# Kernel optimization log

Hardware: AMD Instinct MI355X
Metric: run time of the kernel (lower is better)

The kernel has to match this reference:

```python
import jax, jax.numpy as jnp
import numpy as np

B, S, H, F, G = 8, 2048, 1024, 4096, 128
EPS = 1e-5


def setup_inputs() -> dict:
    key = jax.random.key(0)
    ks = jax.random.split(key, 8)
    x = jax.random.normal(ks[0], (B, S, H), dtype=jnp.float32)
    ln_gamma = jnp.ones((H,), jnp.float32)
    ln_beta = jnp.zeros((H,), jnp.float32)
    # int8-style quantized weights stored as int32 in [0, 256) with zero-point 128
    fc1_q = jax.random.randint(ks[1], (H, F), 0, 256, dtype=jnp.int32)
    fc2_q = jax.random.randint(ks[2], (F, H), 0, 256, dtype=jnp.int32)
    # per-group scales (one scale per 128 rows of K, per output column)
    fc1_scales = jax.random.uniform(ks[3], (H // G, F), jnp.float32) * 0.02 + 0.001
    fc2_scales = jax.random.uniform(ks[4], (F // G, H), jnp.float32) * 0.02 + 0.001
    fc1_bias = jax.random.normal(ks[5], (F,), jnp.float32) * 0.02
    fc2_bias = jax.random.normal(ks[6], (H,), jnp.float32) * 0.02
    return {"x": x, "ln_gamma": ln_gamma, "ln_beta": ln_beta,
            "fc1_q": fc1_q, "fc1_scales": fc1_scales, "fc1_bias": fc1_bias,
            "fc2_q": fc2_q, "fc2_scales": fc2_scales, "fc2_bias": fc2_bias}


def _dequant(q, scales, g):
    # q: [K, N] int, scales: [K//g, N]; zero-point 128 symmetric int8 scheme
    K, N = q.shape
    w = (q.astype(jnp.float32) - 128.0).reshape(K // g, g, N) * scales[:, None, :]
    return w.reshape(K, N)


def reference(x, ln_gamma, ln_beta, fc1_q, fc1_scales, fc1_bias, fc2_q, fc2_scales, fc2_bias):
    residual = x
    # LayerNorm over last dim
    mu = jnp.mean(x, axis=-1, keepdims=True)
    var = jnp.mean(jnp.square(x - mu), axis=-1, keepdims=True)
    h = (x - mu) * jax.lax.rsqrt(var + EPS) * ln_gamma + ln_beta
    hf = h.reshape(-1, H)                       # [B*S, H]
    w1 = _dequant(fc1_q, fc1_scales, G)         # [H, F]
    y = hf @ w1 + fc1_bias                      # [B*S, F]
    y = jax.nn.silu(y)                          # dropout is identity at inference
    w2 = _dequant(fc2_q, fc2_scales, G)         # [F, H]
    z = y @ w2 + fc2_bias                       # [B*S, H]
    return residual + 0.5 * z.reshape(residual.shape)
```

## Files before the change

### kernel.cpp

```cpp
#include <hip/hip_runtime.h>
#include <hip/hip_bf16.h>

#define HH 1024
#define FF 4096
#define MTOT (8 * 2048)

typedef __attribute__((ext_vector_type(4))) float f32x4;
typedef __attribute__((ext_vector_type(8))) short bf16x8;

__device__ inline void async_load16(const void* g, void* l) {
    __builtin_amdgcn_global_load_lds(
        (const __attribute__((address_space(1))) unsigned int*)g,
        (__attribute__((address_space(3))) unsigned int*)l, 16, 0, 0);
}
__device__ inline unsigned lds_off(void* p) {
    return (unsigned)(size_t)(__attribute__((address_space(3))) char*)p;
}
template<int OFF>
__device__ inline bf16x8 dsr(unsigned addr) {
    bf16x8 r;
    asm volatile("ds_read_b128 %0, %1 offset:%2" : "=v"(r) : "v"(addr), "n"(OFF));
    return r;
}
#define SBAR() do { asm volatile("s_barrier" ::: "memory"); __builtin_amdgcn_sched_barrier(0); } while (0)
#define LGKM0() do { asm volatile("s_waitcnt lgkmcnt(0)" ::: "memory"); \
                     __builtin_amdgcn_sched_barrier(0); } while (0)
#define WAIT_VM4() asm volatile("s_waitcnt vmcnt(4)" ::: "memory")
#define WAIT_VM0() asm volatile("s_waitcnt vmcnt(0)" ::: "memory")

template<int BUF, int MH>
__device__ inline void ldA(bf16x8 (&d)[4][2], unsigned vA0, unsigned vA1) {
    constexpr int B = BUF * 32768 + MH * 8192;
    d[0][0] = dsr<B + 0>(vA0);     d[0][1] = dsr<B + 0>(vA1);
    d[1][0] = dsr<B + 2048>(vA0);  d[1][1] = dsr<B + 2048>(vA1);
    d[2][0] = dsr<B + 4096>(vA0);  d[2][1] = dsr<B + 4096>(vA1);
    d[3][0] = dsr<B + 6144>(vA0);  d[3][1] = dsr<B + 6144>(vA1);
}
template<int BUF, int NH>
__device__ inline void ldB(bf16x8 (&d)[2][2], unsigned vB0, unsigned vB1) {
    constexpr int B = BUF * 32768 + NH * 4096;
    d[0][0] = dsr<B + 0>(vB0);     d[0][1] = dsr<B + 0>(vB1);
    d[1][0] = dsr<B + 2048>(vB0);  d[1][1] = dsr<B + 2048>(vB1);
}

__global__ void dequant_t_kernel(const int* __restrict__ q,
                                 const float* __restrict__ scales,
                                 __hip_bfloat16* __restrict__ wt,
                                 int K, int N)
{
    __shared__ float tile[32][33];
    const int n0 = blockIdx.x * 32, k0 = blockIdx.y * 32;
    const int tx = threadIdx.x, ty = threadIdx.y;
#pragma unroll
    for (int i = 0; i < 32; i += 8) {
        int k = k0 + ty + i, n = n0 + tx;
        float s = scales[(size_t)(k >> 7) * N + n];
        tile[ty + i][tx] = (float)(q[(size_t)k * N + n] - 128) * s;
    }
    __syncthreads();
#pragma unroll
    for (int i = 0; i < 32; i += 8) {
        int n = n0 + ty + i, k = k0 + tx;
        wt[(size_t)n * K + k] = __float2bfloat16(tile[tx][ty + i]);
    }
}

__global__ __launch_bounds__(256)
void ln_kernel(const float* __restrict__ x, const float* __restrict__ gamma,
               const float* __restrict__ beta, __hip_bfloat16* __restrict__ hf,
               int m0)
{
    const int row = m0 + blockIdx.x;
    const float4 v = ((const float4*)(x + (size_t)row * HH))[threadIdx.x];
    float s  = v.x + v.y + v.z + v.w;
    float ss = v.x * v.x + v.y * v.y + v.z * v.z + v.w * v.w;
#pragma unroll
    for (int o = 32; o > 0; o >>= 1) { s += __shfl_down(s, o); ss += __shfl_down(ss, o); }
    __shared__ float red[8];
    const int wid = threadIdx.x >> 6, lane = threadIdx.x & 63;
    if (lane == 0) { red[wid] = s; red[4 + wid] = ss; }
    __syncthreads();
    if (threadIdx.x == 0) {
        red[0] = red[0] + red[1] + red[2] + red[3];
        red[4] = red[4] + red[5] + red[6] + red[7];
    }
    __syncthreads();
    const float mu   = red[0] * (1.f / HH);
    const float rstd = rsqrtf(red[4] * (1.f / HH) - mu * mu + 1e-5f);
    const float4 g = ((const float4*)gamma)[threadIdx.x];
    const float4 b = ((const float4*)beta)[threadIdx.x];
    float h0 = (v.x - mu) * rstd * g.x + b.x;
    float h1 = (v.y - mu) * rstd * g.y + b.y;
    float h2 = (v.z - mu) * rstd * g.z + b.z;
    float h3 = (v.w - mu) * rstd * g.w + b.w;
    __hip_bfloat16 t0 = __float2bfloat16(h0), t1 = __float2bfloat16(h1);
    __hip_bfloat16 t2 = __float2bfloat16(h2), t3 = __float2bfloat16(h3);
    ushort4 o;
    o.x = *(unsigned short*)&t0; o.y = *(unsigned short*)&t1;
    o.z = *(unsigned short*)&t2; o.w = *(unsigned short*)&t3;
    ((ushort4*)(hf + (size_t)blockIdx.x * HH))[threadIdx.x] = o;
}

template<int EPI, int KK>
__global__ __launch_bounds__(512, 2)
void gemm256(const __hip_bfloat16* __restrict__ A,
             const __hip_bfloat16* __restrict__ Bt,
             const float* __restrict__ bias,
             const float* __restrict__ resid,
             void* __restrict__ outv,
             int N, int nbx)
{
    __shared__ __align__(16) short As[2][256 * 64];
    __shared__ __align__(16) short Bs[2][256 * 64];
    constexpr int NT = KK >> 6;

    const int nwg = (int)gridDim.x, b = (int)blockIdx.x;
    const int q = nwg >> 3, r = nwg & 7;
    const int xcd = b & 7, pos = b >> 3;
    const int bid = (xcd < r) ? xcd * (q + 1) + pos
                              : r * (q + 1) + (xcd - r) * q + pos;
    const int bx = bid % nbx, by = bid / nbx;
    const int rowA0 = by * 256, colB0 = bx * 256;

    const int tid = (int)threadIdx.x;
    const int lane = tid & 63, wid = tid >> 6;
    const int wr = wid >> 2, wc = wid & 3;
    const int lrow = lane & 15, kg = lane >> 4;
    const int swz = lrow & 7;

    const int srow = tid >> 3;
    const int sgs  = (tid & 7) ^ (srow & 7);
    const __hip_bfloat16* aSrc = A  + (size_t)(rowA0 + srow) * KK + sgs * 8;
    const __hip_bfloat16* bSrc = Bt + (size_t)(colB0 + srow) * KK + sgs * 8;
    short* aDst = &As[0][0] + srow * 64 + (tid & 7) * 8;
    short* bDst = &Bs[0][0] + srow * 64 + (tid & 7) * 8;

    const unsigned asB = lds_off(&As[0][0]);
    const unsigned bsB = lds_off(&Bs[0][0]);
    const unsigned k0off = (unsigned)((kg ^ swz) << 4);
    const unsigned k1off = (unsigned)(((4 + kg) ^ swz) << 4);
    const unsigned vA0 = asB + (unsigned)((wr * 128 + lrow) * 128) + k0off;
    const unsigned vA1 = asB + (unsigned)((wr * 128 + lrow) * 128) + k1off;
    const unsigned vB0 = bsB + (unsigned)((wc * 64 + lrow) * 128) + k0off;
    const unsigned vB1 = bsB + (unsigned)((wc * 64 + lrow) * 128) + k1off;

    auto stA = [&](int buf, int t, int half) {
        const int tt = (t < NT) ? t : NT - 1;
        const size_t ko = (size_t)tt * 64;
        short* d = aDst + buf * 16384 + half * 8192;
        const __hip_bfloat16* s0 = aSrc + (size_t)(half * 128) * KK + ko;
        async_load16(s0, d);
        async_load16(s0 + (size_t)64 * KK, d + 4096);
    };
    auto stB = [&](int buf, int t, int half) {
        const int tt = (t < NT) ? t : NT - 1;
        const size_t ko = (size_t)tt * 64;
        short* d = bDst + buf * 16384 + half * 8192;
        const __hip_bfloat16* s0 = bSrc + (size_t)(half * 128) * KK + ko;
        async_load16(s0, d);
        async_load16(s0 + (size_t)64 * KK, d + 4096);
    };

    f32x4 acc[8][4] = {};
    auto mf = [&](const bf16x8 (&a)[4][2], const bf16x8 (&bb)[2][2], int mh, int nh) {
        __builtin_amdgcn_s_setprio(1);
#pragma unroll
        for (int m2 = 0; m2 < 4; ++m2)
#pragma unroll
            for (int n2 = 0; n2 < 2; ++n2)
#pragma unroll
                for (int ks = 0; ks < 2; ++ks)
                    acc[mh * 4 + m2][nh * 2 + n2] =
                        __builtin_amdgcn_mfma_f32_16x16x32_bf16(
                            a[m2][ks], bb[n2][ks], acc[mh * 4 + m2][nh * 2 + n2], 0, 0, 0);
        __builtin_amdgcn_s_setprio(0);
    };

    stB(0, 0, 0); stB(0, 0, 1); stA(0, 0, 0); stA(0, 0, 1);
    stB(1, 1, 0); stB(1, 1, 1);
    WAIT_VM4();
    SBAR();

    bf16x8 a0[4][2], a1[4][2], b0[2][2], b1[2][2];
    const int NI = NT >> 1;
    for (int i = 0; i < NI; ++i) {
        const int c = 2 * i, n = 2 * i + 1;
        ldA<0, 0>(a0, vA0, vA1); ldB<0, 0>(b0, vB0, vB1);
        stA(1, n, 0);
        SBAR(); LGKM0();
        mf(a0, b0, 0, 0);
        SBAR();
        ldB<0, 1>(b1, vB0, vB1);
        stA(1, n, 1);
        SBAR(); LGKM0();
        mf(a0, b1, 0, 1);
        SBAR();
        ldA<0, 1>(a1, vA0, vA1);
        stB(0, c + 2, 0);
        SBAR(); LGKM0();
        mf(a1, b0, 1, 0);
        SBAR();
        stB(0, c + 2, 1);
        WAIT_VM4();
        SBAR();
        mf(a1, b1, 1, 1);
        SBAR();
        ldA<1, 0>(a0, vA0, vA1); ldB<1, 0>(b0, vB0, vB1);
        stA(0, c + 2, 0);
        SBAR(); LGKM0();
        mf(a0, b0, 0, 0);
        SBAR();
        ldB<1, 1>(b1, vB0, vB1);
        stA(0, c + 2, 1);
        SBAR(); LGKM0();
        mf(a0, b1, 0, 1);
        SBAR();
        ldA<1, 1>(a1, vA0, vA1);
        stB(1, n + 2, 0);
        SBAR(); LGKM0();
        mf(a1, b0, 1, 0);
        SBAR();
        stB(1, n + 2, 1);
        WAIT_VM4();
        SBAR();
        mf(a1, b1, 1, 1);
        SBAR();
    }
    WAIT_VM0();

#pragma unroll
    for (int ni = 0; ni < 4; ++ni) {
        const int col = colB0 + wc * 64 + ni * 16 + lrow;
        const float bv = bias[col];
#pragma unroll
        for (int mi = 0; mi < 8; ++mi) {
            const int row0 = rowA0 + wr * 128 + mi * 16 + kg * 4;
#pragma unroll
            for (int j = 0; j < 4; ++j) {
                const float v = acc[mi][ni][j] + bv;
                const size_t idx = (size_t)(row0 + j) * N + col;
                if (EPI == 0) {
                    const float sv = v / (1.f + __expf(-v));
                    ((__hip_bfloat16*)outv)[idx] = __float2bfloat16(sv);
                } else {
                    ((float*)outv)[idx] = resid[idx] + 0.5f * v;
                }
            }
        }
    }
}

extern "C" void kernel_launch(void* const* d_in, const int* in_sizes, int n_in,
                              void* d_out, int out_size, void* d_ws, size_t ws_size,
                              hipStream_t stream)
{
    const float* x      = (const float*)d_in[0];
    const float* gamma  = (const float*)d_in[1];
    const float* beta   = (const float*)d_in[2];
    const int*   fc1_q  = (const int*)d_in[3];
    const float* fc1_s  = (const float*)d_in[4];
    const float* fc1_b  = (const float*)d_in[5];
    const int*   fc2_q  = (const int*)d_in[6];
    const float* fc2_s  = (const float*)d_in[7];
    const float* fc2_b  = (const float*)d_in[8];
    float* out = (float*)d_out;

    char* ws = (char*)d_ws;
    __hip_bfloat16* w1t = (__hip_bfloat16*)ws;
    __hip_bfloat16* w2t = (__hip_bfloat16*)(ws + (size_t)FF * HH * 2);
    char* dyn = ws + (size_t)2 * FF * HH * 2;
    const size_t avail = ws_size - (size_t)2 * FF * HH * 2;

    int MC = (int)(avail / ((size_t)(HH + FF) * 2));
    MC = (MC / 256) * 256;
    if (MC > MTOT) MC = MTOT;
    if (MC < 256)  MC = 256;

    __hip_bfloat16* hf_c = (__hip_bfloat16*)dyn;
    __hip_bfloat16* y_c  = (__hip_bfloat16*)(dyn + (size_t)MC * HH * 2);

    dequant_t_kernel<<<dim3(FF / 32, HH / 32), dim3(32, 8), 0, stream>>>(
        fc1_q, fc1_s, w1t, HH, FF);
    dequant_t_kernel<<<dim3(HH / 32, FF / 32), dim3(32, 8), 0, stream>>>(
        fc2_q, fc2_s, w2t, FF, HH);

    for (int m0 = 0; m0 < MTOT; m0 += MC) {
        const int mc = (MTOT - m0 < MC) ? (MTOT - m0) : MC;
        ln_kernel<<<mc, 256, 0, stream>>>(x, gamma, beta, hf_c, m0);
        gemm256<0, HH><<<dim3((FF / 256) * (mc / 256)), 512, 0, stream>>>(
            hf_c, w1t, fc1_b, nullptr, (void*)y_c, FF, FF / 256);
        gemm256<1, FF><<<dim3((HH / 256) * (mc / 256)), 512, 0, stream>>>(
            y_c, w2t, fc2_b, x + (size_t)m0 * HH, (void*)(out + (size_t)m0 * HH),
            HH, HH / 256);
    }
}
```

Baseline: 342.0 us.

## Prefetch LDS fragments one phase ahead with partial lgkmcnt waits

Restructures the GEMM main loop so each phase issues the LDS reads for the next phase's fragments before running the current MFMA block. The full lgkmcnt(0) waits become partial waits (4, 8, 0), so LDS latency overlaps with matrix math instead of stalling before every MFMA group. The first fragment loads are hoisted before the loop and the last iteration skips its prefetch. The MFMA loop order is also changed so the k-slice is the outer loop. This relies on exact lgkm counting and on the fragment registers not being overwritten while still in use, and it may raise register pressure.

```diff
diff --git a/kernel.cpp b/kernel.cpp
--- a/kernel.cpp
+++ b/kernel.cpp
@@ -23,8 +23,11 @@
     return r;
 }
 #define SBAR() do { asm volatile("s_barrier" ::: "memory"); __builtin_amdgcn_sched_barrier(0); } while (0)
-#define LGKM0() do { asm volatile("s_waitcnt lgkmcnt(0)" ::: "memory"); \
-                     __builtin_amdgcn_sched_barrier(0); } while (0)
+template<int N>
+__device__ inline void LGKM() {
+    asm volatile("s_waitcnt lgkmcnt(%0)" :: "n"(N) : "memory");
+    __builtin_amdgcn_sched_barrier(0);
+}
 #define WAIT_VM4() asm volatile("s_waitcnt vmcnt(4)" ::: "memory")
 #define WAIT_VM0() asm volatile("s_waitcnt vmcnt(0)" ::: "memory")
 
@@ -165,11 +168,11 @@
     auto mf = [&](const bf16x8 (&a)[4][2], const bf16x8 (&bb)[2][2], int mh, int nh) {
         __builtin_amdgcn_s_setprio(1);
 #pragma unroll
-        for (int m2 = 0; m2 < 4; ++m2)
-#pragma unroll
-            for (int n2 = 0; n2 < 2; ++n2)
-#pragma unroll
-                for (int ks = 0; ks < 2; ++ks)
+        for (int ks = 0; ks < 2; ++ks)
+#pragma unroll
+            for (int m2 = 0; m2 < 4; ++m2)
+#pragma unroll
+                for (int n2 = 0; n2 < 2; ++n2)
                     acc[mh * 4 + m2][nh * 2 + n2] =
                         __builtin_amdgcn_mfma_f32_16x16x32_bf16(
                             a[m2][ks], bb[n2][ks], acc[mh * 4 + m2][nh * 2 + n2], 0, 0, 0);
@@ -180,49 +183,57 @@
     stB(1, 1, 0); stB(1, 1, 1);
     WAIT_VM4();
     SBAR();
-
     bf16x8 a0[4][2], a1[4][2], b0[2][2], b1[2][2];
+    ldA<0, 0>(a0, vA0, vA1);
+    ldB<0, 0>(b0, vB0, vB1);
+
     const int NI = NT >> 1;
     for (int i = 0; i < NI; ++i) {
         const int c = 2 * i, n = 2 * i + 1;
-        ldA<0, 0>(a0, vA0, vA1); ldB<0, 0>(b0, vB0, vB1);
+        ldB<0, 1>(b1, vB0, vB1);
         stA(1, n, 0);
-        SBAR(); LGKM0();
+        SBAR(); LGKM<4>();
         mf(a0, b0, 0, 0);
         SBAR();
-        ldB<0, 1>(b1, vB0, vB1);
+        ldA<0, 1>(a1, vA0, vA1);
         stA(1, n, 1);
-        SBAR(); LGKM0();
+        SBAR(); LGKM<8>();
         mf(a0, b1, 0, 1);
         SBAR();
-        ldA<0, 1>(a1, vA0, vA1);
         stB(0, c + 2, 0);
-        SBAR(); LGKM0();
+        SBAR(); LGKM<0>();
         mf(a1, b0, 1, 0);
         SBAR();
         stB(0, c + 2, 1);
         WAIT_VM4();
         SBAR();
+        ldA<1, 0>(a0, vA0, vA1);
+        ldB<1, 0>(b0, vB0, vB1);
+        __builtin_amdgcn_sched_barrier(0);
         mf(a1, b1, 1, 1);
         SBAR();
-        ldA<1, 0>(a0, vA0, vA1); ldB<1, 0>(b0, vB0, vB1);
+        ldB<1, 1>(b1, vB0, vB1);
         stA(0, c + 2, 0);
-        SBAR(); LGKM0();
+        SBAR(); LGKM<4>();
         mf(a0, b0, 0, 0);
         SBAR();
-        ldB<1, 1>(b1, vB0, vB1);
+        ldA<1, 1>(a1, vA0, vA1);
         stA(0, c + 2, 1);
-        SBAR(); LGKM0();
+        SBAR(); LGKM<8>();
         mf(a0, b1, 0, 1);
         SBAR();
-        ldA<1, 1>(a1, vA0, vA1);
         stB(1, n + 2, 0);
-        SBAR(); LGKM0();
+        SBAR(); LGKM<0>();
         mf(a1, b0, 1, 0);
         SBAR();
         stB(1, n + 2, 1);
         WAIT_VM4();
         SBAR();
+        if (i < NI - 1) {
+            ldA<0, 0>(a0, vA0, vA1);
+            ldB<0, 0>(b0, vB0, vB1);
+        }
+        __builtin_amdgcn_sched_barrier(0);
         mf(a1, b1, 1, 1);
         SBAR();
     }
```

Measured after the change: 334.3 us. 1.02x faster.

## Restructure GEMM prefetch to full double-buffer with deeper in-flight loads

Applied to the files above, without the earlier changes.

Changes the global-to-LDS prefetch schedule so that both A and B tiles for step t+2 are issued together after the current buffer is consumed. This keeps more loads in flight (vmcnt 8 instead of 4) and skips redundant clamped loads on the last iteration. It also reorders the MFMA loop to put k-step outermost and swaps the barrier macro for the builtin without a sched_barrier. The builtin barrier lets the compiler move code across barriers, which adds a risk of hazards around the inline-asm LDS reads.

```diff
diff --git a/kernel.cpp b/kernel.cpp
--- a/kernel.cpp
+++ b/kernel.cpp
@@ -22,10 +22,10 @@
     asm volatile("ds_read_b128 %0, %1 offset:%2" : "=v"(r) : "v"(addr), "n"(OFF));
     return r;
 }
-#define SBAR() do { asm volatile("s_barrier" ::: "memory"); __builtin_amdgcn_sched_barrier(0); } while (0)
+#define SBAR()  __builtin_amdgcn_s_barrier()
 #define LGKM0() do { asm volatile("s_waitcnt lgkmcnt(0)" ::: "memory"); \
                      __builtin_amdgcn_sched_barrier(0); } while (0)
-#define WAIT_VM4() asm volatile("s_waitcnt vmcnt(4)" ::: "memory")
+#define WAIT_VM8() asm volatile("s_waitcnt vmcnt(8)" ::: "memory")
 #define WAIT_VM0() asm volatile("s_waitcnt vmcnt(0)" ::: "memory")
 
 template<int BUF, int MH>
@@ -145,16 +145,14 @@
     const unsigned vB1 = bsB + (unsigned)((wc * 64 + lrow) * 128) + k1off;
 
     auto stA = [&](int buf, int t, int half) {
-        const int tt = (t < NT) ? t : NT - 1;
-        const size_t ko = (size_t)tt * 64;
+        const size_t ko = (size_t)t * 64;
         short* d = aDst + buf * 16384 + half * 8192;
         const __hip_bfloat16* s0 = aSrc + (size_t)(half * 128) * KK + ko;
         async_load16(s0, d);
         async_load16(s0 + (size_t)64 * KK, d + 4096);
     };
     auto stB = [&](int buf, int t, int half) {
-        const int tt = (t < NT) ? t : NT - 1;
-        const size_t ko = (size_t)tt * 64;
+        const size_t ko = (size_t)t * 64;
         short* d = bDst + buf * 16384 + half * 8192;
         const __hip_bfloat16* s0 = bSrc + (size_t)(half * 128) * KK + ko;
         async_load16(s0, d);
@@ -165,63 +163,59 @@
     auto mf = [&](const bf16x8 (&a)[4][2], const bf16x8 (&bb)[2][2], int mh, int nh) {
         __builtin_amdgcn_s_setprio(1);
 #pragma unroll
-        for (int m2 = 0; m2 < 4; ++m2)
-#pragma unroll
-            for (int n2 = 0; n2 < 2; ++n2)
-#pragma unroll
-                for (int ks = 0; ks < 2; ++ks)
+        for (int ks = 0; ks < 2; ++ks)
+#pragma unroll
+            for (int m2 = 0; m2 < 4; ++m2)
+#pragma unroll
+                for (int n2 = 0; n2 < 2; ++n2)
                     acc[mh * 4 + m2][nh * 2 + n2] =
                         __builtin_amdgcn_mfma_f32_16x16x32_bf16(
                             a[m2][ks], bb[n2][ks], acc[mh * 4 + m2][nh * 2 + n2], 0, 0, 0);
         __builtin_amdgcn_s_setprio(0);
     };
 
-    stB(0, 0, 0); stB(0, 0, 1); stA(0, 0, 0); stA(0, 0, 1);
-    stB(1, 1, 0); stB(1, 1, 1);
-    WAIT_VM4();
+    stA(0, 0, 0); stA(0, 0, 1); stB(0, 0, 0); stB(0, 0, 1);
+    stA(1, 1, 0); stB(1, 1, 0); stA(1, 1, 1); stB(1, 1, 1);
+    WAIT_VM8();
     SBAR();
 
     bf16x8 a0[4][2], a1[4][2], b0[2][2], b1[2][2];
     const int NI = NT >> 1;
     for (int i = 0; i < NI; ++i) {
         const int c = 2 * i, n = 2 * i + 1;
+        const bool last = (i == NI - 1);
         ldA<0, 0>(a0, vA0, vA1); ldB<0, 0>(b0, vB0, vB1);
-        stA(1, n, 0);
         SBAR(); LGKM0();
         mf(a0, b0, 0, 0);
         SBAR();
         ldB<0, 1>(b1, vB0, vB1);
-        stA(1, n, 1);
         SBAR(); LGKM0();
         mf(a0, b1, 0, 1);
         SBAR();
         ldA<0, 1>(a1, vA0, vA1);
-        stB(0, c + 2, 0);
+        if (!last) { stA(0, c + 2, 0); stB(0, c + 2, 0); }
         SBAR(); LGKM0();
         mf(a1, b0, 1, 0);
         SBAR();
-        stB(0, c + 2, 1);
-        WAIT_VM4();
+        if (!last) { stA(0, c + 2, 1); stB(0, c + 2, 1); WAIT_VM8(); }
+        else       { WAIT_VM0(); }
         SBAR();
         mf(a1, b1, 1, 1);
         SBAR();
         ldA<1, 0>(a0, vA0, vA1); ldB<1, 0>(b0, vB0, vB1);
-        stA(0, c + 2, 0);
         SBAR(); LGKM0();
         mf(a0, b0, 0, 0);
         SBAR();
         ldB<1, 1>(b1, vB0, vB1);
-        stA(0, c + 2, 1);
         SBAR(); LGKM0();
         mf(a0, b1, 0, 1);
         SBAR();
         ldA<1, 1>(a1, vA0, vA1);
-        stB(1, n + 2, 0);
+        if (!last) { stA(1, n + 2, 0); stB(1, n + 2, 0); }
         SBAR(); LGKM0();
         mf(a1, b0, 1, 0);
         SBAR();
-        stB(1, n + 2, 1);
-        WAIT_VM4();
+        if (!last) { stA(1, n + 2, 1); stB(1, n + 2, 1); WAIT_VM8(); }
         SBAR();
         mf(a1, b1, 1, 1);
         SBAR();
```

After: 331.4 us. 3.1% less time.
